# Performance work log

Hardware: AMD Instinct MI355X
Metric: run time of the kernel (lower is better)

The kernel has to match this reference:

```python
import jax, jax.numpy as jnp
import numpy as np

B, H, W, NC = 8, 64, 64, 128
INTER = NC // 2
BN_EPS = 1e-4


def setup_inputs() -> dict:
    key = jax.random.key(0)
    ks = jax.random.split(key, 6)
    s_in = 1.0 / np.sqrt(NC)
    s_w = 1.0 / np.sqrt(INTER)
    return {
        "x": jax.random.normal(ks[0], (B, H, W, NC), jnp.float32),
        "theta_w": jax.random.normal(ks[1], (NC, INTER), jnp.float32) * s_in,
        "theta_b": jnp.zeros((INTER,), jnp.float32),
        "phi_w": jax.random.normal(ks[2], (NC, INTER), jnp.float32) * s_in,
        "phi_b": jnp.zeros((INTER,), jnp.float32),
        "g_w": jax.random.normal(ks[3], (NC, INTER), jnp.float32) * s_in,
        "g_b": jnp.zeros((INTER,), jnp.float32),
        "W_w": jax.random.normal(ks[4], (INTER, NC), jnp.float32) * s_w,
        "W_b": jnp.zeros((NC,), jnp.float32),
        "bn_gamma": jnp.ones((NC,), jnp.float32),
        "bn_beta": jnp.zeros((NC,), jnp.float32),
        "bn_mean": jnp.zeros((NC,), jnp.float32),
        "bn_var": jax.random.uniform(ks[5], (NC,), jnp.float32, 0.5, 1.5),
    }


def reference(x, theta_w, theta_b, phi_w, phi_b, g_w, g_b, W_w, W_b,
              bn_gamma, bn_beta, bn_mean, bn_var):
    b, h, w, c = x.shape
    n = h * w
    # 1x1 conv projections == per-pixel GEMMs; flatten spatial to tokens
    xt = x.reshape(b, n, c)                                  # [B, N, C]
    theta = xt @ theta_w + theta_b                           # [B, N, C']
    phi = xt @ phi_w + phi_b                                 # [B, N, C']
    g = xt @ g_w + g_b                                       # [B, N, C']
    # single-head, unscaled non-local attention
    f = jnp.einsum("bnc,bmc->bnm", theta, phi)               # [B, N, N]
    attn = jax.nn.softmax(f, axis=-1)
    y = jnp.einsum("bnm,bmc->bnc", attn, g)                  # [B, N, C']
    # W: 1x1 conv back to nc + BatchNorm (inference), then residual
    wy = y @ W_w + W_b                                       # [B, N, C]
    inv = bn_gamma * jax.lax.rsqrt(bn_var + BN_EPS)
    wy = (wy - bn_mean) * inv + bn_beta
    z = wy.reshape(b, h, w, c) + x
    return z
```

## Files before the change

kernel.cpp:

```cpp
#include <hip/hip_runtime.h>
#include <math.h>

typedef _Float16 v8h __attribute__((ext_vector_type(8)));
typedef float v4f __attribute__((ext_vector_type(4)));
typedef float v16f __attribute__((ext_vector_type(16)));

#define MFMA32(a, b, c) __builtin_amdgcn_mfma_f32_32x32x16_f16((a), (b), (c), 0, 0, 0)
#define MFMA16(a, b, c) __builtin_amdgcn_mfma_f32_16x16x32_f16((a), (b), (c), 0, 0, 0)
#define ZV4 ((v4f){0.f, 0.f, 0.f, 0.f})
#define LOG2E 1.44269504f

#define TA64(row, colb)  ((((row) * 128) + (colb)) ^ (((row) & 7) << 4))
#define TA128(row, colb) ((((row) * 256) + (colb)) ^ (((row) & 15) << 4))

#define RAW_BARRIER() do {                                        \
    asm volatile("s_waitcnt lgkmcnt(0)" ::: "memory");            \
    asm volatile("s_barrier" ::: "memory");                       \
} while (0)

__device__ __forceinline__ unsigned int pk_f16(float a, float b) {
    return __builtin_bit_cast(unsigned int, __builtin_amdgcn_cvt_pkrtz(a, b));
}
__device__ __forceinline__ void pl32swap(unsigned int& a, unsigned int& b) {
    asm("v_permlane32_swap_b32 %0, %1" : "+v"(a), "+v"(b));
}
__device__ __forceinline__ float fexp2(float x) {
    float r;
    asm("v_exp_f32 %0, %1" : "=v"(r) : "v"(x));
    return r;
}

__global__ __launch_bounds__(256) void k_prep(
    const float* __restrict__ tw, const float* __restrict__ pw,
    const float* __restrict__ gw,
    const float* __restrict__ Ww, const float* __restrict__ Wb,
    const float* __restrict__ gamma, const float* __restrict__ beta,
    const float* __restrict__ mean, const float* __restrict__ var,
    _Float16* __restrict__ Wt, _Float16* __restrict__ wallT,
    float* __restrict__ sc, float* __restrict__ bi)
{
    int gid = blockIdx.x * 256 + threadIdx.x;
    #pragma unroll
    for (int r = 0; r < 2; ++r) {
        int idx = r * 4096 + gid;
        int d = idx >> 7, c = idx & 127;
        Wt[c * 64 + d] = (_Float16)Ww[idx];
    }
    #pragma unroll
    for (int r = 0; r < 6; ++r) {
        int idx = r * 4096 + gid;
        int p = idx >> 13, rem = idx & 8191;
        int o = rem >> 7, k = rem & 127;
        const float* wm = (p == 0) ? tw : (p == 1) ? pw : gw;
        wallT[idx] = (_Float16)wm[k * 64 + o];
    }
    if (blockIdx.x == 0 && threadIdx.x < 128) {
        int c = threadIdx.x;
        float inv = gamma[c] * rsqrtf(var[c] + 1e-4f);
        sc[c] = inv;
        bi[c] = (Wb[c] - mean[c]) * inv + beta[c];
    }
}

__global__ __launch_bounds__(512, 4) void k_proj(
    const float* __restrict__ x, const _Float16* __restrict__ wallT,
    const float* __restrict__ tb, const float* __restrict__ pb,
    const float* __restrict__ gb,
    _Float16* __restrict__ theta, _Float16* __restrict__ phi,
    _Float16* __restrict__ gT)
{
    __shared__ __align__(16) _Float16 tsc[8][16 * 72];
    const int t = threadIdx.x;
    const int w = t >> 6, l = t & 63, h = l >> 4, lo = l & 15;
    const int tok0 = blockIdx.x * 128 + w * 16;
    _Float16* tw_l = &tsc[w][0];

    v8h xA[4];
    #pragma unroll
    for (int kc = 0; kc < 4; ++kc) {
        const float* px = x + (size_t)(tok0 + lo) * 128 + kc * 32 + h * 8;
        float4 f0 = *(const float4*)(px);
        float4 f1 = *(const float4*)(px + 4);
        uint4 u;
        u.x = pk_f16(f0.x, f0.y); u.y = pk_f16(f0.z, f0.w);
        u.z = pk_f16(f1.x, f1.y); u.w = pk_f16(f1.z, f1.w);
        xA[kc] = __builtin_bit_cast(v8h, u);
    }

    #pragma unroll
    for (int p = 0; p < 2; ++p) {
        const _Float16* wp = wallT + p * 8192;
        const float* bias = (p == 0) ? tb : pb;
        _Float16* dst = (p == 0) ? theta : phi;
        const float scale = (p == 0) ? LOG2E : 1.0f;
        #pragma unroll
        for (int oc = 0; oc < 4; ++oc) {
            int o = oc * 16 + lo;
            v4f acc = ZV4;
            #pragma unroll
            for (int kc = 0; kc < 4; ++kc) {
                v8h B = *(const v8h*)(wp + o * 128 + kc * 32 + h * 8);
                acc = MFMA16(xA[kc], B, acc);
            }
            float bv = bias[o];
            #pragma unroll
            for (int rr = 0; rr < 4; ++rr)
                tw_l[(4 * h + rr) * 72 + o] = (_Float16)((acc[rr] + bv) * scale);
        }
        int token = l >> 2, c = l & 3;
        v8h v0 = *(const v8h*)&tw_l[token * 72 + c * 16];
        v8h v1 = *(const v8h*)&tw_l[token * 72 + c * 16 + 8];
        _Float16* dp = dst + (size_t)(tok0 + token) * 64 + c * 16;
        *(v8h*)(dp) = v0;
        *(v8h*)(dp + 8) = v1;
    }
    {
        const _Float16* wp = wallT + 2 * 8192;
        int tokg = tok0 + lo;
        int bb = tokg >> 12, n = tokg & 4095;
        #pragma unroll
        for (int oc = 0; oc < 4; ++oc) {
            v4f acc = ZV4;
            #pragma unroll
            for (int kc = 0; kc < 4; ++kc) {
                v8h A = *(const v8h*)(wp + (oc * 16 + lo) * 128 + kc * 32 + h * 8);
                acc = MFMA16(A, xA[kc], acc);
            }
            #pragma unroll
            for (int rr = 0; rr < 4; ++rr) {
                int o = oc * 16 + 4 * h + rr;
                gT[((size_t)bb * 64 + o) * 4096 + n] = (_Float16)(acc[rr] + gb[o]);
            }
        }
    }
}

__global__ __launch_bounds__(512, 4) void k_attn(
    const _Float16* __restrict__ theta,
    const _Float16* __restrict__ phi,
    const _Float16* __restrict__ gT,
    const _Float16* __restrict__ Wt,
    const float* __restrict__ sc, const float* __restrict__ bi,
    const float* __restrict__ x, float* __restrict__ out)
{
    __shared__ __align__(16) _Float16 ldsbuf[32768];
    __shared__ float zf[8 * 32];

    const int t = threadIdx.x;
    const int w = t >> 6, l = t & 63, q32 = l & 31, hi2 = l >> 5;
    const int qt = w & 1, kh = w >> 1;
    const int bid = blockIdx.x;
    const int b = bid & 7, qb = bid >> 3;
    const size_t tok0 = (size_t)b * 4096 + qb * 64;
    const int tokA = (int)(qb * 64) + qt * 32;

    char* phB = (char*)ldsbuf;
    char* gvB = (char*)ldsbuf + 32768;

    v8h thB[4];
    #pragma unroll
    for (int kc = 0; kc < 4; ++kc)
        thB[kc] = *(const v8h*)(theta +
            (tok0 + qt * 32 + q32) * 64 + kc * 16 + hi2 * 8);

    const _Float16* phb = phi + (size_t)b * 4096 * 64;
    const _Float16* gvb = gT + (size_t)b * 64 * 4096;

    v16f yacc[2];
    #pragma unroll
    for (int df = 0; df < 2; ++df)
        #pragma unroll
        for (int r = 0; r < 16; ++r) yacc[df][r] = 0.f;
    float mrow = -INFINITY, lpart = 0.f;

    int qkRd[4], gvRd[2][2];
    #pragma unroll
    for (int kc = 0; kc < 4; ++kc)
        qkRd[kc] = TA64(kh * 32 + q32, (kc * 16 + hi2 * 8) * 2);
    #pragma unroll
    for (int df = 0; df < 2; ++df)
        #pragma unroll
        for (int s = 0; s < 2; ++s)
            gvRd[df][s] = TA128(df * 32 + q32, (kh * 32 + s * 16 + hi2 * 8) * 2);

    const int phA0 = TA64(t >> 3, (t & 7) * 16);
    const int phA1 = TA64((t >> 3) + 64, (t & 7) * 16);
    const int gvA0 = TA128(t >> 4, (t & 15) * 16);
    const int gvA1 = TA128((t >> 4) + 32, (t & 15) * 16);
    const _Float16* pPh = phb + (size_t)(t >> 3) * 64 + (t & 7) * 8;
    const _Float16* pGv = gvb + (size_t)(t >> 4) * 4096 + (t & 15) * 8;

    v8h pf0 = *(const v8h*)(pPh);
    v8h pf1 = *(const v8h*)(pPh + 64 * 64);
    v8h pf2 = *(const v8h*)(pGv);
    v8h pf3 = *(const v8h*)(pGv + (size_t)32 * 4096);
    pPh += 8192; pGv += 128;

    for (int kt = 0; kt < 32; ++kt) {
        char* phL = phB + (kt & 1) * 16384;
        char* gvL = gvB + (kt & 1) * 16384;
        *(v8h*)(phL + phA0) = pf0;
        *(v8h*)(phL + phA1) = pf1;
        *(v8h*)(gvL + gvA0) = pf2;
        *(v8h*)(gvL + gvA1) = pf3;
        if (kt < 31) {
            pf0 = *(const v8h*)(pPh);
            pf1 = *(const v8h*)(pPh + 64 * 64);
            pf2 = *(const v8h*)(pGv);
            pf3 = *(const v8h*)(pGv + (size_t)32 * 4096);
            pPh += 8192; pGv += 128;
        }
        RAW_BARRIER();
        v16f S;
        #pragma unroll
        for (int r = 0; r < 16; ++r) S[r] = 0.f;
        __builtin_amdgcn_s_setprio(1);
        #pragma unroll
        for (int kc = 0; kc < 4; ++kc) {
            v8h A = *(const v8h*)(phL + qkRd[kc]);
            S = MFMA32(A, thB[kc], S);
        }
        __builtin_amdgcn_s_setprio(0);
        float m0 = fmaxf(fmaxf(S[0], S[1]), S[2]);
        float m1 = fmaxf(fmaxf(S[3], S[4]), S[5]);
        float m2 = fmaxf(fmaxf(S[6], S[7]), S[8]);
        float m3 = fmaxf(fmaxf(S[9], S[10]), S[11]);
        float m4 = fmaxf(fmaxf(S[12], S[13]), S[14]);
        float vmax = fmaxf(fmaxf(fmaxf(m0, m1), fmaxf(m2, m3)),
                           fmaxf(m4, S[15]));
        vmax = fmaxf(vmax, __shfl_xor(vmax, 32));
        if (!__all(vmax <= mrow + 11.54f)) {
            float mn = fmaxf(mrow, vmax);
            float aa = fexp2(mrow - mn);
            mrow = mn;
            lpart *= aa;
            #pragma unroll
            for (int df = 0; df < 2; ++df)
                #pragma unroll
                for (int r = 0; r < 16; ++r)
                    yacc[df][r] *= aa;
        }
        float psum = 0.f;
        #pragma unroll
        for (int r = 0; r < 16; ++r) {
            S[r] = fexp2(S[r] - mrow);
            psum += S[r];
        }
        lpart += psum;
        unsigned int W0 = pk_f16(S[0], S[1]),   W1 = pk_f16(S[2], S[3]);
        unsigned int W2 = pk_f16(S[4], S[5]),   W3 = pk_f16(S[6], S[7]);
        unsigned int W4 = pk_f16(S[8], S[9]),   W5 = pk_f16(S[10], S[11]);
        unsigned int W6 = pk_f16(S[12], S[13]), W7 = pk_f16(S[14], S[15]);
        pl32swap(W0, W2); pl32swap(W1, W3);
        pl32swap(W4, W6); pl32swap(W5, W7);
        uint4 ub1; ub1.x = W0; ub1.y = W1; ub1.z = W2; ub1.w = W3;
        uint4 ub2; ub2.x = W4; ub2.y = W5; ub2.z = W6; ub2.w = W7;
        v8h pBv[2] = {__builtin_bit_cast(v8h, ub1), __builtin_bit_cast(v8h, ub2)};
        __builtin_amdgcn_s_setprio(1);
        #pragma unroll
        for (int df = 0; df < 2; ++df)
            #pragma unroll
            for (int s = 0; s < 2; ++s) {
                v8h A = *(const v8h*)(gvL + gvRd[df][s]);
                yacc[df] = MFMA32(A, pBv[s], yacc[df]);
            }
        __builtin_amdgcn_s_setprio(0);
    }

    __syncthreads();
    float lrow = lpart + __shfl_xor(lpart, 32);
    float inv = 1.0f / lrow;
    {
        char* slot = (char*)ldsbuf + w * 4096 + l * 64;
        #pragma unroll
        for (int j = 0; j < 4; ++j) {
            int df = j >> 1, r0 = (j & 1) * 8;
            uint4 u;
            u.x = pk_f16(yacc[df][r0 + 0] * inv, yacc[df][r0 + 1] * inv);
            u.y = pk_f16(yacc[df][r0 + 2] * inv, yacc[df][r0 + 3] * inv);
            u.z = pk_f16(yacc[df][r0 + 4] * inv, yacc[df][r0 + 5] * inv);
            u.w = pk_f16(yacc[df][r0 + 6] * inv, yacc[df][r0 + 7] * inv);
            *(uint4*)(slot + (j * 16 ^ ((l & 3) << 4))) = u;
        }
        zf[w * 32 + q32] = mrow + __log2f(lrow);
    }
    __syncthreads();
    if (w >= 2) return;

    float zq[4];
    #pragma unroll
    for (int kp = 0; kp < 4; ++kp) zq[kp] = zf[(kp * 2 + qt) * 32 + q32];
    float zmx = fmaxf(fmaxf(zq[0], zq[1]), fmaxf(zq[2], zq[3]));
    float wsum = 0.f;
    float yfin[2][16];
    #pragma unroll
    for (int df = 0; df < 2; ++df)
        #pragma unroll
        for (int r = 0; r < 16; ++r) yfin[df][r] = 0.f;
    #pragma unroll
    for (int kp = 0; kp < 4; ++kp) {
        char* slot = (char*)ldsbuf + (kp * 2 + qt) * 4096 + l * 64;
        float wk = fexp2(zq[kp] - zmx);
        wsum += wk;
        #pragma unroll
        for (int j = 0; j < 4; ++j) {
            v8h c = *(const v8h*)(slot + (j * 16 ^ ((l & 3) << 4)));
            int df = j >> 1, r0 = (j & 1) * 8;
            #pragma unroll
            for (int e = 0; e < 8; ++e)
                yfin[df][r0 + e] += wk * (float)c[e];
        }
    }
    float nrm = 1.0f / wsum;
    v8h yA[4];
    #pragma unroll
    for (int kc = 0; kc < 4; ++kc) {
        int df = kc >> 1, r0 = (kc & 1) * 8;
        unsigned int Wa = pk_f16(yfin[df][r0 + 0] * nrm, yfin[df][r0 + 1] * nrm);
        unsigned int Wb2 = pk_f16(yfin[df][r0 + 2] * nrm, yfin[df][r0 + 3] * nrm);
        unsigned int Wc = pk_f16(yfin[df][r0 + 4] * nrm, yfin[df][r0 + 5] * nrm);
        unsigned int Wd = pk_f16(yfin[df][r0 + 6] * nrm, yfin[df][r0 + 7] * nrm);
        pl32swap(Wa, Wc); pl32swap(Wb2, Wd);
        uint4 u; u.x = Wa; u.y = Wb2; u.z = Wc; u.w = Wd;
        yA[kc] = __builtin_bit_cast(v8h, u);
    }
    const float* xb = x + (size_t)b * 4096 * 128;
    float* ob = out + (size_t)b * 4096 * 128;
    #pragma unroll
    for (int cf = 0; cf < 4; ++cf) {
        int c = cf * 32 + q32;
        v16f wy;
        #pragma unroll
        for (int r = 0; r < 16; ++r) wy[r] = 0.f;
        #pragma unroll
        for (int kc = 0; kc < 4; ++kc) {
            v8h wB = *(const v8h*)(Wt + c * 64 + kc * 16 + hi2 * 8);
            wy = MFMA32(yA[kc], wB, wy);
        }
        float scc = sc[c], bic = bi[c];
        #pragma unroll
        for (int r = 0; r < 16; ++r) {
            int qrow = (r & 3) + 8 * (r >> 2) + 4 * hi2;
            size_t off = (size_t)(tokA + qrow) * 128 + c;
            ob[off] = wy[r] * scc + bic + xb[off];
        }
    }
}

extern "C" void kernel_launch(void* const* d_in, const int* in_sizes, int n_in,
                              void* d_out, int out_size, void* d_ws, size_t ws_size,
                              hipStream_t stream) {
    const float* x     = (const float*)d_in[0];
    const float* tw    = (const float*)d_in[1];
    const float* tb    = (const float*)d_in[2];
    const float* pw    = (const float*)d_in[3];
    const float* pb    = (const float*)d_in[4];
    const float* gw    = (const float*)d_in[5];
    const float* gb    = (const float*)d_in[6];
    const float* Ww    = (const float*)d_in[7];
    const float* Wb    = (const float*)d_in[8];
    const float* gamma = (const float*)d_in[9];
    const float* beta  = (const float*)d_in[10];
    const float* mean  = (const float*)d_in[11];
    const float* var   = (const float*)d_in[12];

    char* ws = (char*)d_ws;
    _Float16* theta = (_Float16*)ws;
    _Float16* phi   = (_Float16*)(ws + (4u << 20));
    _Float16* gT    = (_Float16*)(ws + (8u << 20));
    _Float16* Wt    = (_Float16*)(ws + (12u << 20));
    _Float16* wallT = (_Float16*)(ws + (12u << 20) + (1u << 16));
    float* sc       = (float*)(ws + (12u << 20) + (2u << 16));
    float* bi       = sc + 128;

    k_prep<<<16, 256, 0, stream>>>(tw, pw, gw, Ww, Wb, gamma, beta, mean, var,
                                   Wt, wallT, sc, bi);
    k_proj<<<256, 512, 0, stream>>>(x, wallT, tb, pb, gb, theta, phi, gT);
    k_attn<<<512, 512, 0, stream>>>(theta, phi, gT, Wt, sc, bi,
                                    x, (float*)d_out);
}
```

Baseline: 100.3 us.

## Software-pipeline attention loop: phi direct to registers, triple-buffered g, deferred PV

Each wave now loads its phi rows straight from global memory into registers instead of staging them through LDS. The g tile moves to a three-slot LDS ring, which allows one barrier per iteration. The P·V MFMAs for the previous tile are issued right after the current tile's QK MFMAs, so the softmax math overlaps with matrix work. The row sum now uses fdot2 on the packed f16 probabilities, and the occupancy hint drops from 4 to 2 blocks per unit. The aims are fewer LDS writes and reads, fewer barriers and more overlap. The costs are higher register pressure, lower occupancy, and row sums computed from f16-rounded values.

```diff
diff --git a/kernel.cpp b/kernel.cpp
--- a/kernel.cpp
+++ b/kernel.cpp
@@ -2,6 +2,7 @@
 #include <math.h>
 
 typedef _Float16 v8h __attribute__((ext_vector_type(8)));
+typedef __fp16 h2 __attribute__((ext_vector_type(2)));
 typedef float v4f __attribute__((ext_vector_type(4)));
 typedef float v16f __attribute__((ext_vector_type(16)));
 
@@ -135,7 +136,7 @@
     }
 }
 
-__global__ __launch_bounds__(512, 4) void k_attn(
+__global__ __launch_bounds__(512, 2) void k_attn(
     const _Float16* __restrict__ theta,
     const _Float16* __restrict__ phi,
     const _Float16* __restrict__ gT,
@@ -143,7 +144,7 @@
     const float* __restrict__ sc, const float* __restrict__ bi,
     const float* __restrict__ x, float* __restrict__ out)
 {
-    __shared__ __align__(16) _Float16 ldsbuf[32768];
+    __shared__ __align__(16) _Float16 gvbuf[3 * 8192];
     __shared__ float zf[8 * 32];
 
     const int t = threadIdx.x;
@@ -154,8 +155,9 @@
     const size_t tok0 = (size_t)b * 4096 + qb * 64;
     const int tokA = (int)(qb * 64) + qt * 32;
 
-    char* phB = (char*)ldsbuf;
-    char* gvB = (char*)ldsbuf + 32768;
+    char* gv0 = (char*)gvbuf;
+    char* gv1 = (char*)gvbuf + 16384;
+    char* gv2 = (char*)gvbuf + 32768;
 
     v8h thB[4];
     #pragma unroll
@@ -173,53 +175,110 @@
         for (int r = 0; r < 16; ++r) yacc[df][r] = 0.f;
     float mrow = -INFINITY, lpart = 0.f;
 
-    int qkRd[4], gvRd[2][2];
-    #pragma unroll
-    for (int kc = 0; kc < 4; ++kc)
-        qkRd[kc] = TA64(kh * 32 + q32, (kc * 16 + hi2 * 8) * 2);
+    int gvRd[2][2];
     #pragma unroll
     for (int df = 0; df < 2; ++df)
         #pragma unroll
         for (int s = 0; s < 2; ++s)
             gvRd[df][s] = TA128(df * 32 + q32, (kh * 32 + s * 16 + hi2 * 8) * 2);
 
-    const int phA0 = TA64(t >> 3, (t & 7) * 16);
-    const int phA1 = TA64((t >> 3) + 64, (t & 7) * 16);
     const int gvA0 = TA128(t >> 4, (t & 15) * 16);
     const int gvA1 = TA128((t >> 4) + 32, (t & 15) * 16);
-    const _Float16* pPh = phb + (size_t)(t >> 3) * 64 + (t & 7) * 8;
     const _Float16* pGv = gvb + (size_t)(t >> 4) * 4096 + (t & 15) * 8;
-
-    v8h pf0 = *(const v8h*)(pPh);
-    v8h pf1 = *(const v8h*)(pPh + 64 * 64);
-    v8h pf2 = *(const v8h*)(pGv);
-    v8h pf3 = *(const v8h*)(pGv + (size_t)32 * 4096);
-    pPh += 8192; pGv += 128;
-
-    for (int kt = 0; kt < 32; ++kt) {
-        char* phL = phB + (kt & 1) * 16384;
-        char* gvL = gvB + (kt & 1) * 16384;
-        *(v8h*)(phL + phA0) = pf0;
-        *(v8h*)(phL + phA1) = pf1;
-        *(v8h*)(gvL + gvA0) = pf2;
-        *(v8h*)(gvL + gvA1) = pf3;
+    const _Float16* pPhi = phb + (size_t)(kh * 32 + q32) * 64 + hi2 * 8;
+
+    v8h gW0, gW1, gN0, gN1;
+    {
+        v8h a0 = *(const v8h*)(pGv);
+        v8h a1 = *(const v8h*)(pGv + (size_t)32 * 4096);
+        *(v8h*)(gv0 + gvA0) = a0;
+        *(v8h*)(gv0 + gvA1) = a1;
+        v8h b0 = *(const v8h*)(pGv + 128);
+        v8h b1 = *(const v8h*)(pGv + 128 + (size_t)32 * 4096);
+        *(v8h*)(gv1 + gvA0) = b0;
+        *(v8h*)(gv1 + gvA1) = b1;
+        gW0 = *(const v8h*)(pGv + 256);
+        gW1 = *(const v8h*)(pGv + 256 + (size_t)32 * 4096);
+    }
+    v8h pc0 = *(const v8h*)(pPhi +  0), pc1 = *(const v8h*)(pPhi + 16);
+    v8h pc2 = *(const v8h*)(pPhi + 32), pc3 = *(const v8h*)(pPhi + 48);
+    v8h pn0 = *(const v8h*)(pPhi + 8192 +  0), pn1 = *(const v8h*)(pPhi + 8192 + 16);
+    v8h pn2 = *(const v8h*)(pPhi + 8192 + 32), pn3 = *(const v8h*)(pPhi + 8192 + 48);
+    __syncthreads();
+
+    unsigned int Pp[8];
+    {
+        v16f S = {};
+        S = MFMA32(pc0, thB[0], S); S = MFMA32(pc1, thB[1], S);
+        S = MFMA32(pc2, thB[2], S); S = MFMA32(pc3, thB[3], S);
+        float m0 = fmaxf(fmaxf(S[0], S[1]), S[2]);
+        float m1 = fmaxf(fmaxf(S[3], S[4]), S[5]);
+        float m2 = fmaxf(fmaxf(S[6], S[7]), S[8]);
+        float m3 = fmaxf(fmaxf(S[9], S[10]), S[11]);
+        float m4 = fmaxf(fmaxf(S[12], S[13]), S[14]);
+        float vmax = fmaxf(fmaxf(fmaxf(m0, m1), fmaxf(m2, m3)),
+                           fmaxf(m4, S[15]));
+        vmax = fmaxf(vmax, __shfl_xor(vmax, 32));
+        mrow = vmax;
+        const h2 one2 = {(__fp16)1.0f, (__fp16)1.0f};
+        float psum = 0.f;
+        h2 pk[8];
+        #pragma unroll
+        for (int r = 0; r < 16; ++r) S[r] = fexp2(S[r] - mrow);
+        #pragma unroll
+        for (int j = 0; j < 8; ++j) {
+            pk[j] = __builtin_amdgcn_cvt_pkrtz(S[2 * j], S[2 * j + 1]);
+            psum = __builtin_amdgcn_fdot2(pk[j], one2, psum, false);
+        }
+        lpart = psum;
+        unsigned int W0 = __builtin_bit_cast(unsigned int, pk[0]);
+        unsigned int W1 = __builtin_bit_cast(unsigned int, pk[1]);
+        unsigned int W2 = __builtin_bit_cast(unsigned int, pk[2]);
+        unsigned int W3 = __builtin_bit_cast(unsigned int, pk[3]);
+        unsigned int W4 = __builtin_bit_cast(unsigned int, pk[4]);
+        unsigned int W5 = __builtin_bit_cast(unsigned int, pk[5]);
+        unsigned int W6 = __builtin_bit_cast(unsigned int, pk[6]);
+        unsigned int W7 = __builtin_bit_cast(unsigned int, pk[7]);
+        pl32swap(W0, W2); pl32swap(W1, W3);
+        pl32swap(W4, W6); pl32swap(W5, W7);
+        Pp[0] = W0; Pp[1] = W1; Pp[2] = W2; Pp[3] = W3;
+        Pp[4] = W4; Pp[5] = W5; Pp[6] = W6; Pp[7] = W7;
+    }
+    pc0 = pn0; pc1 = pn1; pc2 = pn2; pc3 = pn3;
+
+    int bR = 0, bW = 2;
+    char* gvBufs[3] = {gv0, gv1, gv2};
+
+    for (int kt = 1; kt < 32; ++kt) {
+        if (kt < 30) {
+            gN0 = *(const v8h*)(pGv + (kt + 2) * 128);
+            gN1 = *(const v8h*)(pGv + (kt + 2) * 128 + (size_t)32 * 4096);
+        }
         if (kt < 31) {
-            pf0 = *(const v8h*)(pPh);
-            pf1 = *(const v8h*)(pPh + 64 * 64);
-            pf2 = *(const v8h*)(pGv);
-            pf3 = *(const v8h*)(pGv + (size_t)32 * 4096);
-            pPh += 8192; pGv += 128;
+            const _Float16* pp = pPhi + (size_t)(kt + 1) * 8192;
+            pn0 = *(const v8h*)(pp +  0); pn1 = *(const v8h*)(pp + 16);
+            pn2 = *(const v8h*)(pp + 32); pn3 = *(const v8h*)(pp + 48);
         }
         RAW_BARRIER();
-        v16f S;
-        #pragma unroll
-        for (int r = 0; r < 16; ++r) S[r] = 0.f;
+        char* bufR = gvBufs[bR];
+        char* bufW = gvBufs[bW];
+        if (kt < 31) {
+            *(v8h*)(bufW + gvA0) = gW0;
+            *(v8h*)(bufW + gvA1) = gW1;
+        }
+        v16f S = {};
         __builtin_amdgcn_s_setprio(1);
-        #pragma unroll
-        for (int kc = 0; kc < 4; ++kc) {
-            v8h A = *(const v8h*)(phL + qkRd[kc]);
-            S = MFMA32(A, thB[kc], S);
-        }
+        S = MFMA32(pc0, thB[0], S); S = MFMA32(pc1, thB[1], S);
+        S = MFMA32(pc2, thB[2], S); S = MFMA32(pc3, thB[3], S);
+        #pragma unroll
+        for (int df = 0; df < 2; ++df)
+            #pragma unroll
+            for (int s = 0; s < 2; ++s) {
+                v8h A = *(const v8h*)(bufR + gvRd[df][s]);
+                v8h pB = __builtin_bit_cast(v8h,
+                    *(uint4*)&Pp[s * 4]);
+                yacc[df] = MFMA32(A, pB, yacc[df]);
+            }
         __builtin_amdgcn_s_setprio(0);
         float m0 = fmaxf(fmaxf(S[0], S[1]), S[2]);
         float m1 = fmaxf(fmaxf(S[3], S[4]), S[5]);
@@ -240,38 +299,51 @@
                 for (int r = 0; r < 16; ++r)
                     yacc[df][r] *= aa;
         }
+        #pragma unroll
+        for (int r = 0; r < 16; ++r) S[r] = fexp2(S[r] - mrow);
+        const h2 one2 = {(__fp16)1.0f, (__fp16)1.0f};
         float psum = 0.f;
-        #pragma unroll
-        for (int r = 0; r < 16; ++r) {
-            S[r] = fexp2(S[r] - mrow);
-            psum += S[r];
+        h2 pk[8];
+        #pragma unroll
+        for (int j = 0; j < 8; ++j) {
+            pk[j] = __builtin_amdgcn_cvt_pkrtz(S[2 * j], S[2 * j + 1]);
+            psum = __builtin_amdgcn_fdot2(pk[j], one2, psum, false);
         }
         lpart += psum;
-        unsigned int W0 = pk_f16(S[0], S[1]),   W1 = pk_f16(S[2], S[3]);
-        unsigned int W2 = pk_f16(S[4], S[5]),   W3 = pk_f16(S[6], S[7]);
-        unsigned int W4 = pk_f16(S[8], S[9]),   W5 = pk_f16(S[10], S[11]);
-        unsigned int W6 = pk_f16(S[12], S[13]), W7 = pk_f16(S[14], S[15]);
+        unsigned int W0 = __builtin_bit_cast(unsigned int, pk[0]);
+        unsigned int W1 = __builtin_bit_cast(unsigned int, pk[1]);
+        unsigned int W2 = __builtin_bit_cast(unsigned int, pk[2]);
+        unsigned int W3 = __builtin_bit_cast(unsigned int, pk[3]);
+        unsigned int W4 = __builtin_bit_cast(unsigned int, pk[4]);
+        unsigned int W5 = __builtin_bit_cast(unsigned int, pk[5]);
+        unsigned int W6 = __builtin_bit_cast(unsigned int, pk[6]);
+        unsigned int W7 = __builtin_bit_cast(unsigned int, pk[7]);
         pl32swap(W0, W2); pl32swap(W1, W3);
         pl32swap(W4, W6); pl32swap(W5, W7);
-        uint4 ub1; ub1.x = W0; ub1.y = W1; ub1.z = W2; ub1.w = W3;
-        uint4 ub2; ub2.x = W4; ub2.y = W5; ub2.z = W6; ub2.w = W7;
-        v8h pBv[2] = {__builtin_bit_cast(v8h, ub1), __builtin_bit_cast(v8h, ub2)};
-        __builtin_amdgcn_s_setprio(1);
+        Pp[0] = W0; Pp[1] = W1; Pp[2] = W2; Pp[3] = W3;
+        Pp[4] = W4; Pp[5] = W5; Pp[6] = W6; Pp[7] = W7;
+        pc0 = pn0; pc1 = pn1; pc2 = pn2; pc3 = pn3;
+        gW0 = gN0; gW1 = gN1;
+        bR = (bR == 2) ? 0 : bR + 1;
+        bW = (bW == 2) ? 0 : bW + 1;
+    }
+    {
+        char* bufR = gvBufs[bR];
         #pragma unroll
         for (int df = 0; df < 2; ++df)
             #pragma unroll
             for (int s = 0; s < 2; ++s) {
-                v8h A = *(const v8h*)(gvL + gvRd[df][s]);
-                yacc[df] = MFMA32(A, pBv[s], yacc[df]);
+                v8h A = *(const v8h*)(bufR + gvRd[df][s]);
+                v8h pB = __builtin_bit_cast(v8h, *(uint4*)&Pp[s * 4]);
+                yacc[df] = MFMA32(A, pB, yacc[df]);
             }
-        __builtin_amdgcn_s_setprio(0);
     }
 
     __syncthreads();
     float lrow = lpart + __shfl_xor(lpart, 32);
     float inv = 1.0f / lrow;
     {
-        char* slot = (char*)ldsbuf + w * 4096 + l * 64;
+        char* slot = (char*)gvbuf + w * 4096 + l * 64;
         #pragma unroll
         for (int j = 0; j < 4; ++j) {
             int df = j >> 1, r0 = (j & 1) * 8;
@@ -299,7 +371,7 @@
         for (int r = 0; r < 16; ++r) yfin[df][r] = 0.f;
     #pragma unroll
     for (int kp = 0; kp < 4; ++kp) {
-        char* slot = (char*)ldsbuf + (kp * 2 + qt) * 4096 + l * 64;
+        char* slot = (char*)gvbuf + (kp * 2 + qt) * 4096 + l * 64;
         float wk = fexp2(zq[kp] - zmx);
         wsum += wk;
         #pragma unroll
@@ -329,9 +401,7 @@
     #pragma unroll
     for (int cf = 0; cf < 4; ++cf) {
         int c = cf * 32 + q32;
-        v16f wy;
-        #pragma unroll
-        for (int r = 0; r < 16; ++r) wy[r] = 0.f;
+        v16f wy = {};
         #pragma unroll
         for (int kc = 0; kc < 4; ++kc) {
             v8h wB = *(const v8h*)(Wt + c * 64 + kc * 16 + hi2 * 8);
```

Measured after the change: 117.8 us. 1.17x slower.

## Load phi straight to registers, stage gT stores through LDS, pack softmax sums

Applied to the files above, without the earlier changes.

The attention kernel no longer stages phi tiles through shared memory. Each wave loads its phi MFMA operands directly from global memory into registers, prefetched one tile ahead, which halves LDS traffic and the LDS footprint. The projection kernel now transposes g through an LDS block so gT is written with coalesced 16-byte stores. The softmax row sum is computed with packed f16 dot products over the already-converted probabilities. Launch bounds for k_attn drop to 2 blocks per SM, allowing more registers at the cost of occupancy, and the phi global reads are now repeated across waves.

```diff
diff --git a/kernel.cpp b/kernel.cpp
--- a/kernel.cpp
+++ b/kernel.cpp
@@ -2,6 +2,7 @@
 #include <math.h>
 
 typedef _Float16 v8h __attribute__((ext_vector_type(8)));
+typedef __fp16 h2 __attribute__((ext_vector_type(2)));
 typedef float v4f __attribute__((ext_vector_type(4)));
 typedef float v16f __attribute__((ext_vector_type(16)));
 
@@ -10,7 +11,6 @@
 #define ZV4 ((v4f){0.f, 0.f, 0.f, 0.f})
 #define LOG2E 1.44269504f
 
-#define TA64(row, colb)  ((((row) * 128) + (colb)) ^ (((row) & 7) << 4))
 #define TA128(row, colb) ((((row) * 256) + (colb)) ^ (((row) & 15) << 4))
 
 #define RAW_BARRIER() do {                                        \
@@ -70,6 +70,7 @@
     _Float16* __restrict__ gT)
 {
     __shared__ __align__(16) _Float16 tsc[8][16 * 72];
+    __shared__ __align__(16) _Float16 gblk[64][136];
     const int t = threadIdx.x;
     const int w = t >> 6, l = t & 63, h = l >> 4, lo = l & 15;
     const int tok0 = blockIdx.x * 128 + w * 16;
@@ -116,8 +117,6 @@
     }
     {
         const _Float16* wp = wallT + 2 * 8192;
-        int tokg = tok0 + lo;
-        int bb = tokg >> 12, n = tokg & 4095;
         #pragma unroll
         for (int oc = 0; oc < 4; ++oc) {
             v4f acc = ZV4;
@@ -129,13 +128,24 @@
             #pragma unroll
             for (int rr = 0; rr < 4; ++rr) {
                 int o = oc * 16 + 4 * h + rr;
-                gT[((size_t)bb * 64 + o) * 4096 + n] = (_Float16)(acc[rr] + gb[o]);
+                gblk[o][w * 16 + lo] = (_Float16)(acc[rr] + gb[o]);
             }
         }
     }
-}
-
-__global__ __launch_bounds__(512, 4) void k_attn(
+    __syncthreads();
+    {
+        int o = t >> 3, ch = t & 7;
+        v8h v0 = *(const v8h*)&gblk[o][ch * 16];
+        v8h v1 = *(const v8h*)&gblk[o][ch * 16 + 8];
+        int tokg0 = blockIdx.x * 128;
+        int bb = tokg0 >> 12, n0 = (tokg0 & 4095) + ch * 16;
+        _Float16* gp = gT + ((size_t)bb * 64 + o) * 4096 + n0;
+        *(v8h*)(gp) = v0;
+        *(v8h*)(gp + 8) = v1;
+    }
+}
+
+__global__ __launch_bounds__(512, 2) void k_attn(
     const _Float16* __restrict__ theta,
     const _Float16* __restrict__ phi,
     const _Float16* __restrict__ gT,
@@ -143,7 +153,7 @@
     const float* __restrict__ sc, const float* __restrict__ bi,
     const float* __restrict__ x, float* __restrict__ out)
 {
-    __shared__ __align__(16) _Float16 ldsbuf[32768];
+    __shared__ __align__(16) _Float16 gvbuf[2 * 8192];
     __shared__ float zf[8 * 32];
 
     const int t = threadIdx.x;
@@ -154,9 +164,6 @@
     const size_t tok0 = (size_t)b * 4096 + qb * 64;
     const int tokA = (int)(qb * 64) + qt * 32;
 
-    char* phB = (char*)ldsbuf;
-    char* gvB = (char*)ldsbuf + 32768;
-
     v8h thB[4];
     #pragma unroll
     for (int kc = 0; kc < 4; ++kc)
@@ -173,53 +180,42 @@
         for (int r = 0; r < 16; ++r) yacc[df][r] = 0.f;
     float mrow = -INFINITY, lpart = 0.f;
 
-    int qkRd[4], gvRd[2][2];
-    #pragma unroll
-    for (int kc = 0; kc < 4; ++kc)
-        qkRd[kc] = TA64(kh * 32 + q32, (kc * 16 + hi2 * 8) * 2);
+    int gvRd[2][2];
     #pragma unroll
     for (int df = 0; df < 2; ++df)
         #pragma unroll
         for (int s = 0; s < 2; ++s)
             gvRd[df][s] = TA128(df * 32 + q32, (kh * 32 + s * 16 + hi2 * 8) * 2);
 
-    const int phA0 = TA64(t >> 3, (t & 7) * 16);
-    const int phA1 = TA64((t >> 3) + 64, (t & 7) * 16);
     const int gvA0 = TA128(t >> 4, (t & 15) * 16);
     const int gvA1 = TA128((t >> 4) + 32, (t & 15) * 16);
-    const _Float16* pPh = phb + (size_t)(t >> 3) * 64 + (t & 7) * 8;
     const _Float16* pGv = gvb + (size_t)(t >> 4) * 4096 + (t & 15) * 8;
-
-    v8h pf0 = *(const v8h*)(pPh);
-    v8h pf1 = *(const v8h*)(pPh + 64 * 64);
-    v8h pf2 = *(const v8h*)(pGv);
-    v8h pf3 = *(const v8h*)(pGv + (size_t)32 * 4096);
-    pPh += 8192; pGv += 128;
+    const _Float16* pPhi = phb + (size_t)(kh * 32 + q32) * 64 + hi2 * 8;
+
+    v8h gW0 = *(const v8h*)(pGv);
+    v8h gW1 = *(const v8h*)(pGv + (size_t)32 * 4096);
+    v8h pc0 = *(const v8h*)(pPhi +  0), pc1 = *(const v8h*)(pPhi + 16);
+    v8h pc2 = *(const v8h*)(pPhi + 32), pc3 = *(const v8h*)(pPhi + 48);
+    v8h pn0 = *(const v8h*)(pPhi + 8192 +  0), pn1 = *(const v8h*)(pPhi + 8192 + 16);
+    v8h pn2 = *(const v8h*)(pPhi + 8192 + 32), pn3 = *(const v8h*)(pPhi + 8192 + 48);
+    v8h gN0, gN1;
 
     for (int kt = 0; kt < 32; ++kt) {
-        char* phL = phB + (kt & 1) * 16384;
-        char* gvL = gvB + (kt & 1) * 16384;
-        *(v8h*)(phL + phA0) = pf0;
-        *(v8h*)(phL + phA1) = pf1;
-        *(v8h*)(gvL + gvA0) = pf2;
-        *(v8h*)(gvL + gvA1) = pf3;
+        char* buf = (char*)gvbuf + (kt & 1) * 16384;
+        *(v8h*)(buf + gvA0) = gW0;
+        *(v8h*)(buf + gvA1) = gW1;
         if (kt < 31) {
-            pf0 = *(const v8h*)(pPh);
-            pf1 = *(const v8h*)(pPh + 64 * 64);
-            pf2 = *(const v8h*)(pGv);
-            pf3 = *(const v8h*)(pGv + (size_t)32 * 4096);
-            pPh += 8192; pGv += 128;
+            gN0 = *(const v8h*)(pGv + (size_t)(kt + 1) * 128);
+            gN1 = *(const v8h*)(pGv + (size_t)(kt + 1) * 128 + (size_t)32 * 4096);
+            const _Float16* pp = pPhi + (size_t)(kt + 1) * 8192;
+            pn0 = *(const v8h*)(pp +  0); pn1 = *(const v8h*)(pp + 16);
+            pn2 = *(const v8h*)(pp + 32); pn3 = *(const v8h*)(pp + 48);
         }
         RAW_BARRIER();
-        v16f S;
-        #pragma unroll
-        for (int r = 0; r < 16; ++r) S[r] = 0.f;
+        v16f S = {};
         __builtin_amdgcn_s_setprio(1);
-        #pragma unroll
-        for (int kc = 0; kc < 4; ++kc) {
-            v8h A = *(const v8h*)(phL + qkRd[kc]);
-            S = MFMA32(A, thB[kc], S);
-        }
+        S = MFMA32(pc0, thB[0], S); S = MFMA32(pc1, thB[1], S);
+        S = MFMA32(pc2, thB[2], S); S = MFMA32(pc3, thB[3], S);
         __builtin_amdgcn_s_setprio(0);
         float m0 = fmaxf(fmaxf(S[0], S[1]), S[2]);
         float m1 = fmaxf(fmaxf(S[3], S[4]), S[5]);
@@ -240,38 +236,49 @@
                 for (int r = 0; r < 16; ++r)
                     yacc[df][r] *= aa;
         }
+        #pragma unroll
+        for (int r = 0; r < 16; ++r) S[r] = fexp2(S[r] - mrow);
+        const h2 one2 = {(__fp16)1.0f, (__fp16)1.0f};
         float psum = 0.f;
-        #pragma unroll
-        for (int r = 0; r < 16; ++r) {
-            S[r] = fexp2(S[r] - mrow);
-            psum += S[r];
+        h2 pk[8];
+        #pragma unroll
+        for (int j = 0; j < 8; ++j) {
+            pk[j] = __builtin_amdgcn_cvt_pkrtz(S[2 * j], S[2 * j + 1]);
+            psum = __builtin_amdgcn_fdot2(pk[j], one2, psum, false);
         }
         lpart += psum;
-        unsigned int W0 = pk_f16(S[0], S[1]),   W1 = pk_f16(S[2], S[3]);
-        unsigned int W2 = pk_f16(S[4], S[5]),   W3 = pk_f16(S[6], S[7]);
-        unsigned int W4 = pk_f16(S[8], S[9]),   W5 = pk_f16(S[10], S[11]);
-        unsigned int W6 = pk_f16(S[12], S[13]), W7 = pk_f16(S[14], S[15]);
+        unsigned int W0 = __builtin_bit_cast(unsigned int, pk[0]);
+        unsigned int W1 = __builtin_bit_cast(unsigned int, pk[1]);
+        unsigned int W2 = __builtin_bit_cast(unsigned int, pk[2]);
+        unsigned int W3 = __builtin_bit_cast(unsigned int, pk[3]);
+        unsigned int W4 = __builtin_bit_cast(unsigned int, pk[4]);
+        unsigned int W5 = __builtin_bit_cast(unsigned int, pk[5]);
+        unsigned int W6 = __builtin_bit_cast(unsigned int, pk[6]);
+        unsigned int W7 = __builtin_bit_cast(unsigned int, pk[7]);
         pl32swap(W0, W2); pl32swap(W1, W3);
         pl32swap(W4, W6); pl32swap(W5, W7);
         uint4 ub1; ub1.x = W0; ub1.y = W1; ub1.z = W2; ub1.w = W3;
         uint4 ub2; ub2.x = W4; ub2.y = W5; ub2.z = W6; ub2.w = W7;
-        v8h pBv[2] = {__builtin_bit_cast(v8h, ub1), __builtin_bit_cast(v8h, ub2)};
+        v8h pB1 = __builtin_bit_cast(v8h, ub1);
+        v8h pB2 = __builtin_bit_cast(v8h, ub2);
         __builtin_amdgcn_s_setprio(1);
         #pragma unroll
-        for (int df = 0; df < 2; ++df)
-            #pragma unroll
-            for (int s = 0; s < 2; ++s) {
-                v8h A = *(const v8h*)(gvL + gvRd[df][s]);
-                yacc[df] = MFMA32(A, pBv[s], yacc[df]);
-            }
+        for (int df = 0; df < 2; ++df) {
+            v8h A0 = *(const v8h*)(buf + gvRd[df][0]);
+            v8h A1 = *(const v8h*)(buf + gvRd[df][1]);
+            yacc[df] = MFMA32(A0, pB1, yacc[df]);
+            yacc[df] = MFMA32(A1, pB2, yacc[df]);
+        }
         __builtin_amdgcn_s_setprio(0);
+        pc0 = pn0; pc1 = pn1; pc2 = pn2; pc3 = pn3;
+        gW0 = gN0; gW1 = gN1;
     }
 
     __syncthreads();
     float lrow = lpart + __shfl_xor(lpart, 32);
     float inv = 1.0f / lrow;
     {
-        char* slot = (char*)ldsbuf + w * 4096 + l * 64;
+        char* slot = (char*)gvbuf + w * 4096 + l * 64;
         #pragma unroll
         for (int j = 0; j < 4; ++j) {
             int df = j >> 1, r0 = (j & 1) * 8;
@@ -299,7 +306,7 @@
         for (int r = 0; r < 16; ++r) yfin[df][r] = 0.f;
     #pragma unroll
     for (int kp = 0; kp < 4; ++kp) {
-        char* slot = (char*)ldsbuf + (kp * 2 + qt) * 4096 + l * 64;
+        char* slot = (char*)gvbuf + (kp * 2 + qt) * 4096 + l * 64;
         float wk = fexp2(zq[kp] - zmx);
         wsum += wk;
         #pragma unroll
@@ -329,9 +336,7 @@
     #pragma unroll
     for (int cf = 0; cf < 4; ++cf) {
         int c = cf * 32 + q32;
-        v16f wy;
-        #pragma unroll
-        for (int r = 0; r < 16; ++r) wy[r] = 0.f;
+        v16f wy = {};
         #pragma unroll
         for (int kc = 0; kc < 4; ++kc) {
             v8h wB = *(const v8h*)(Wt + c * 64 + kc * 16 + hi2 * 8);
```

Result: slower. 103.3 us (+2.9%).
